# Optimization experiments

Hardware: AMD Instinct MI355X
Metric: run time of the kernel (lower is better)

## Reference

```python
import jax, jax.numpy as jnp
import numpy as np

T, IN, H, OUT = 4096, 2048, 2048, 1


def setup_inputs() -> dict:
    key = jax.random.key(0)
    ks = jax.random.split(key, 7)
    s = 0.02  # small init scale to keep gates in a sane range
    return {
        "x": jax.random.normal(ks[0], (T, 1, IN), dtype=jnp.float32),
        "W_ih": s * jax.random.normal(ks[1], (4 * H, IN), dtype=jnp.float32),
        "W_hh": s * jax.random.normal(ks[2], (4 * H, H), dtype=jnp.float32),
        "b_ih": s * jax.random.normal(ks[3], (4 * H,), dtype=jnp.float32),
        "b_hh": s * jax.random.normal(ks[4], (4 * H,), dtype=jnp.float32),
        "W_out": s * jax.random.normal(ks[5], (OUT, H), dtype=jnp.float32),
        "b_out": s * jax.random.normal(ks[6], (OUT,), dtype=jnp.float32),
    }


def reference(x, W_ih, W_hh, b_ih, b_hh, W_out, b_out):
    # Faithful LSTMCell loop (PyTorch gate order i, f, g, o) + per-step Linear.
    hidden = W_hh.shape[1]

    def step(carry, x_t):  # x_t: [1, IN]
        h, c = carry
        gates = x_t @ W_ih.T + b_ih + h @ W_hh.T + b_hh  # [1, 4H]
        i, f, g, o = jnp.split(gates, 4, axis=-1)
        i = jax.nn.sigmoid(i)
        f = jax.nn.sigmoid(f)
        g = jnp.tanh(g)
        o = jax.nn.sigmoid(o)
        c = f * c + i * g
        h = o * jnp.tanh(c)
        y = (h @ W_out.T + b_out)[0, 0]  # scalar, output_size == 1
        return (h, c), y

    h0 = jnp.zeros((1, hidden), dtype=x.dtype)
    c0 = jnp.zeros((1, hidden), dtype=x.dtype)
    _, res = jax.lax.scan(step, (h0, c0), x)
    return res  # [T]
```

## Files before the change

kernel.cpp:

```cpp
#include <hip/hip_runtime.h>

#define T_STEPS 4096
#define HD 2048
#define G4 8192
#define NWG 256
#define NTH 1024
#define SENT 0x7FC0DEADu

typedef __attribute__((ext_vector_type(8))) short bf16x8;
typedef __attribute__((ext_vector_type(4))) float f32x4;
typedef __attribute__((ext_vector_type(2))) float f32x2;
typedef __attribute__((ext_vector_type(8))) unsigned short u16x8;

static __device__ __forceinline__ unsigned short f2bf(float f){
  union { float f; unsigned int u; } v; v.f = f;
  unsigned int r = (v.u + 0x7fffu + ((v.u >> 16) & 1u)) >> 16;
  return (unsigned short)r;
}
static __device__ __forceinline__ float bf2f(unsigned short s){
  union { unsigned int u; float f; } v; v.u = ((unsigned int)s) << 16;
  return v.f;
}

static __device__ __forceinline__ f32x2 ld2_uc(const float* p){
  f32x2 r;
  asm volatile("global_load_dwordx2 %0, %1, off sc0 sc1\n\ts_waitcnt vmcnt(0)"
               : "=v"(r) : "v"(p) : "memory");
  return r;
}
static __device__ __forceinline__ void st_uc(float* p, float v){
  asm volatile("global_store_dword %0, %1, off sc0 sc1" :: "v"(p), "v"(v) : "memory");
}

__global__ void init_kernel(const float* __restrict__ b_ih, const float* __restrict__ b_hh,
                            float* __restrict__ bias, float* __restrict__ Hbuf){
  int i = blockIdx.x*blockDim.x + threadIdx.x;
  int stride = gridDim.x*blockDim.x;
  const int NTOT = G4 + (T_STEPS+1)*HD;
  union { unsigned int u; float f; } sent; sent.u = SENT;
  for (int idx = i; idx < NTOT; idx += stride){
    if (idx < G4) bias[idx] = b_ih[idx] + b_hh[idx];
    else {
      int j = idx - G4;
      Hbuf[j] = (j < HD) ? 0.f : sent.f;
    }
  }
}

__global__ __launch_bounds__(256) void gemm_xp(const float* __restrict__ X,
                                               const float* __restrict__ W,
                                               const float* __restrict__ bias,
                                               unsigned short* __restrict__ XP){
  __shared__ __align__(16) unsigned short As[128][40];
  __shared__ __align__(16) unsigned short Bs[128][40];
  const int tid = threadIdx.x;
  const int bx = blockIdx.x & 63;
  const int by = blockIdx.x >> 6;
  const int row0 = by*128, col0 = bx*128;
  const int l = tid & 63, w = tid >> 6;
  const int wrow = (w>>1)*64, wcol = (w&1)*64;
  const int lr = l & 15, lk = l >> 4;

  f32x4 acc[4][4];
  #pragma unroll
  for (int mi=0; mi<4; mi++)
    #pragma unroll
    for (int ni=0; ni<4; ni++)
      acc[mi][ni] = (f32x4){0.f,0.f,0.f,0.f};

  const int sr = tid >> 1;
  const int sh = (tid & 1) * 16;
  const float* xb = X + (size_t)(row0+sr)*2048 + sh;
  const float* wb = W + (size_t)(col0+sr)*2048 + sh;

  for (int k0 = 0; k0 < 2048; k0 += 32){
    __syncthreads();
    u16x8 va[2], vb[2];
    #pragma unroll
    for (int q=0; q<2; q++){
      float4 u = *(const float4*)(xb + k0 + q*8);
      float4 v = *(const float4*)(xb + k0 + q*8 + 4);
      u16x8 t;
      t[0]=f2bf(u.x); t[1]=f2bf(u.y); t[2]=f2bf(u.z); t[3]=f2bf(u.w);
      t[4]=f2bf(v.x); t[5]=f2bf(v.y); t[6]=f2bf(v.z); t[7]=f2bf(v.w);
      va[q]=t;
      float4 p = *(const float4*)(wb + k0 + q*8);
      float4 r = *(const float4*)(wb + k0 + q*8 + 4);
      u16x8 s;
      s[0]=f2bf(p.x); s[1]=f2bf(p.y); s[2]=f2bf(p.z); s[3]=f2bf(p.w);
      s[4]=f2bf(r.x); s[5]=f2bf(r.y); s[6]=f2bf(r.z); s[7]=f2bf(r.w);
      vb[q]=s;
    }
    *(u16x8*)&As[sr][sh]   = va[0];
    *(u16x8*)&As[sr][sh+8] = va[1];
    *(u16x8*)&Bs[sr][sh]   = vb[0];
    *(u16x8*)&Bs[sr][sh+8] = vb[1];
    __syncthreads();

    bf16x8 af[4], bfr[4];
    #pragma unroll
    for (int mi=0; mi<4; mi++) af[mi]  = *(const bf16x8*)&As[wrow+mi*16+lr][lk*8];
    #pragma unroll
    for (int ni=0; ni<4; ni++) bfr[ni] = *(const bf16x8*)&Bs[wcol+ni*16+lr][lk*8];
    #pragma unroll
    for (int mi=0; mi<4; mi++)
      #pragma unroll
      for (int ni=0; ni<4; ni++)
        acc[mi][ni] = __builtin_amdgcn_mfma_f32_16x16x32_bf16(af[mi], bfr[ni], acc[mi][ni], 0,0,0);
  }

  #pragma unroll
  for (int ni=0; ni<4; ni++){
    const int jc = col0 + wcol + ni*16 + lr;
    const float bv = bias[jc];
    #pragma unroll
    for (int mi=0; mi<4; mi++){
      const int tr0 = row0 + wrow + mi*16 + lk*4;
      #pragma unroll
      for (int r=0; r<4; r++)
        XP[(size_t)(tr0+r)*G4 + jc] = f2bf(acc[mi][ni][r] + bv);
    }
  }
}

__global__ __launch_bounds__(NTH, 4) void recur(const unsigned short* __restrict__ XP,
                                                const float* __restrict__ Whh,
                                                float* __restrict__ Hbuf){
  __shared__ float h_lds[HD];
  __shared__ float gsum[32];
  __shared__ float xp_s[32];
  const int g = blockIdx.x;
  const int tid = threadIdx.x;
  const int l = tid & 63, w = tid >> 6;

  float wv[2][8][4];
  #pragma unroll
  for (int ri=0; ri<2; ri++){
    const int rr = 2*w + ri;
    const size_t jrow = (size_t)(rr>>3)*HD + g*8 + (rr&7);
    const float* wp = Whh + jrow*HD + l*4;
    #pragma unroll
    for (int c=0; c<8; c++){
      float4 t4 = *(const float4*)(wp + c*256);
      wv[ri][c][0]=t4.x; wv[ri][c][1]=t4.y; wv[ri][c][2]=t4.z; wv[ri][c][3]=t4.w;
      asm volatile("" : "+v"(wv[ri][c][0]), "+v"(wv[ri][c][1]),
                        "+v"(wv[ri][c][2]), "+v"(wv[ri][c][3]));
    }
  }

  float c_reg = 0.f;

  for (int t=0; t<T_STEPS; ++t){
    if (tid < 32)
      xp_s[tid] = bf2f(XP[(size_t)t*G4 + (size_t)(tid>>3)*HD + g*8 + (tid&7)]);

    const float* hp = Hbuf + (size_t)t*HD + tid*2;
    f32x2 hv;
    do {
      hv = ld2_uc(hp);
    } while (__float_as_uint(hv[0]) == SENT || __float_as_uint(hv[1]) == SENT);
    *(f32x2*)&h_lds[tid*2] = hv;
    __syncthreads();

    float a0 = 0.f, a1 = 0.f;
    #pragma unroll
    for (int c=0; c<8; c++){
      float4 h4 = *(const float4*)&h_lds[c*256 + l*4];
      a0 += wv[0][c][0]*h4.x + wv[0][c][1]*h4.y + wv[0][c][2]*h4.z + wv[0][c][3]*h4.w;
      a1 += wv[1][c][0]*h4.x + wv[1][c][1]*h4.y + wv[1][c][2]*h4.z + wv[1][c][3]*h4.w;
    }
    #pragma unroll
    for (int off=32; off; off>>=1){
      a0 += __shfl_xor(a0, off, 64);
      a1 += __shfl_xor(a1, off, 64);
    }
    if (l == 0){ gsum[2*w] = a0; gsum[2*w+1] = a1; }
    __syncthreads();

    if (tid < 8){
      float ipre = gsum[tid]    + xp_s[tid];
      float fpre = gsum[8+tid]  + xp_s[8+tid];
      float gpre = gsum[16+tid] + xp_s[16+tid];
      float opre = gsum[24+tid] + xp_s[24+tid];
      float iv = 1.f/(1.f + __expf(-ipre));
      float fv = 1.f/(1.f + __expf(-fpre));
      float e2 = __expf(-2.f*gpre);
      float gv = (1.f - e2)/(1.f + e2);
      float ov = 1.f/(1.f + __expf(-opre));
      c_reg = fv*c_reg + iv*gv;
      float e2c = __expf(-2.f*c_reg);
      float th = (1.f - e2c)/(1.f + e2c);
      st_uc(Hbuf + (size_t)(t+1)*HD + g*8 + tid, ov*th);
    }
  }
}

__global__ __launch_bounds__(256) void out_gemv(const float* __restrict__ Hbuf,
                                                const float* __restrict__ Wout,
                                                const float* __restrict__ bout,
                                                float* __restrict__ y){
  const int t = blockIdx.x;
  const int tid = threadIdx.x;
  const float* h = Hbuf + (size_t)(t+1)*HD;
  float4 a0 = *(const float4*)(h + tid*8);
  float4 a1 = *(const float4*)(h + tid*8 + 4);
  float4 w0 = *(const float4*)(Wout + tid*8);
  float4 w1 = *(const float4*)(Wout + tid*8 + 4);
  float s = a0.x*w0.x + a0.y*w0.y + a0.z*w0.z + a0.w*w0.w
          + a1.x*w1.x + a1.y*w1.y + a1.z*w1.z + a1.w*w1.w;
  #pragma unroll
  for (int off=32; off; off>>=1) s += __shfl_xor(s, off, 64);
  __shared__ float ps[4];
  if ((tid & 63) == 0) ps[tid>>6] = s;
  __syncthreads();
  if (tid == 0) y[t] = ps[0]+ps[1]+ps[2]+ps[3] + bout[0];
}

extern "C" void kernel_launch(void* const* d_in, const int* in_sizes, int n_in,
                              void* d_out, int out_size, void* d_ws, size_t ws_size,
                              hipStream_t stream) {
  const float* x    = (const float*)d_in[0];
  const float* Wih  = (const float*)d_in[1];
  const float* Whh  = (const float*)d_in[2];
  const float* b_ih = (const float*)d_in[3];
  const float* b_hh = (const float*)d_in[4];
  const float* Wout = (const float*)d_in[5];
  const float* bout = (const float*)d_in[6];
  float* y = (float*)d_out;

  char* ws = (char*)d_ws;
  unsigned short* XP = (unsigned short*)(ws);
  float* Hbuf        = (float*)(ws + 67108864);
  float* bias        = (float*)(ws + 100671488);

  init_kernel<<<2048, 256, 0, stream>>>(b_ih, b_hh, bias, Hbuf);
  gemm_xp<<<2048, 256, 0, stream>>>(x, Wih, bias, XP);

  void* args[] = {(void*)&XP, (void*)&Whh, (void*)&Hbuf};
  hipLaunchCooperativeKernel((void*)recur, dim3(NWG), dim3(NTH), args, 0, stream);

  out_gemv<<<T_STEPS, 256, 0, stream>>>(Hbuf, Wout, bout, y);
}
```

Before: 10.53 ms.

## Store recurrent weights as bf16 in LDS instead of fp32 registers

```diff
diff --git a/kernel.cpp b/kernel.cpp
--- a/kernel.cpp
+++ b/kernel.cpp
@@ -6,6 +6,7 @@
 #define NWG 256
 #define NTH 1024
 #define SENT 0x7FC0DEADu
+#define SMEM_BYTES (131072 + 8192 + 128)
 
 typedef __attribute__((ext_vector_type(8))) short bf16x8;
 typedef __attribute__((ext_vector_type(4))) float f32x4;
@@ -20,6 +21,12 @@
 static __device__ __forceinline__ float bf2f(unsigned short s){
   union { unsigned int u; float f; } v; v.u = ((unsigned int)s) << 16;
   return v.f;
+}
+static __device__ __forceinline__ float blo(unsigned int u){
+  return __uint_as_float(u << 16);
+}
+static __device__ __forceinline__ float bhi(unsigned int u){
+  return __uint_as_float(u & 0xffff0000u);
 }
 
 static __device__ __forceinline__ f32x2 ld2_uc(const float* p){
@@ -126,34 +133,40 @@
 __global__ __launch_bounds__(NTH, 4) void recur(const unsigned short* __restrict__ XP,
                                                 const float* __restrict__ Whh,
                                                 float* __restrict__ Hbuf){
-  __shared__ float h_lds[HD];
-  __shared__ float gsum[32];
-  __shared__ float xp_s[32];
+  extern __shared__ char smem[];
+  float* h_lds = (float*)(smem + 131072);
+  float* gsum  = (float*)(smem + 131072 + 8192);
   const int g = blockIdx.x;
   const int tid = threadIdx.x;
   const int l = tid & 63, w = tid >> 6;
 
-  float wv[2][8][4];
   #pragma unroll
   for (int ri=0; ri<2; ri++){
     const int rr = 2*w + ri;
-    const size_t jrow = (size_t)(rr>>3)*HD + g*8 + (rr&7);
+    const size_t jrow = (size_t)(rr>>3)*HD + (size_t)g*8 + (rr&7);
     const float* wp = Whh + jrow*HD + l*4;
     #pragma unroll
-    for (int c=0; c<8; c++){
-      float4 t4 = *(const float4*)(wp + c*256);
-      wv[ri][c][0]=t4.x; wv[ri][c][1]=t4.y; wv[ri][c][2]=t4.z; wv[ri][c][3]=t4.w;
-      asm volatile("" : "+v"(wv[ri][c][0]), "+v"(wv[ri][c][1]),
-                        "+v"(wv[ri][c][2]), "+v"(wv[ri][c][3]));
+    for (int cp=0; cp<4; cp++){
+      float4 fa = *(const float4*)(wp + (2*cp)*256);
+      float4 fb = *(const float4*)(wp + (2*cp+1)*256);
+      uint4 pk;
+      pk.x = ((unsigned)f2bf(fa.y)<<16) | f2bf(fa.x);
+      pk.y = ((unsigned)f2bf(fa.w)<<16) | f2bf(fa.z);
+      pk.z = ((unsigned)f2bf(fb.y)<<16) | f2bf(fb.x);
+      pk.w = ((unsigned)f2bf(fb.w)<<16) | f2bf(fb.z);
+      *(uint4*)(smem + (size_t)((ri*4+cp)*1024 + tid)*16) = pk;
     }
   }
 
   float c_reg = 0.f;
+  float xpv[4] = {0,0,0,0};
 
   for (int t=0; t<T_STEPS; ++t){
-    if (tid < 32)
-      xp_s[tid] = bf2f(XP[(size_t)t*G4 + (size_t)(tid>>3)*HD + g*8 + (tid&7)]);
-
+    if (tid < 8){
+      #pragma unroll
+      for (int q=0; q<4; q++)
+        xpv[q] = bf2f(XP[(size_t)t*G4 + (size_t)q*HD + g*8 + tid]);
+    }
     const float* hp = Hbuf + (size_t)t*HD + tid*2;
     f32x2 hv;
     do {
@@ -164,10 +177,15 @@
 
     float a0 = 0.f, a1 = 0.f;
     #pragma unroll
-    for (int c=0; c<8; c++){
-      float4 h4 = *(const float4*)&h_lds[c*256 + l*4];
-      a0 += wv[0][c][0]*h4.x + wv[0][c][1]*h4.y + wv[0][c][2]*h4.z + wv[0][c][3]*h4.w;
-      a1 += wv[1][c][0]*h4.x + wv[1][c][1]*h4.y + wv[1][c][2]*h4.z + wv[1][c][3]*h4.w;
+    for (int cp=0; cp<4; cp++){
+      float4 ha = *(const float4*)&h_lds[(2*cp)*256 + l*4];
+      float4 hb = *(const float4*)&h_lds[(2*cp+1)*256 + l*4];
+      uint4 w0 = *(const uint4*)(smem + (size_t)((cp  )*1024 + tid)*16);
+      uint4 w1 = *(const uint4*)(smem + (size_t)((4+cp)*1024 + tid)*16);
+      a0 += blo(w0.x)*ha.x + bhi(w0.x)*ha.y + blo(w0.y)*ha.z + bhi(w0.y)*ha.w
+          + blo(w0.z)*hb.x + bhi(w0.z)*hb.y + blo(w0.w)*hb.z + bhi(w0.w)*hb.w;
+      a1 += blo(w1.x)*ha.x + bhi(w1.x)*ha.y + blo(w1.y)*ha.z + bhi(w1.y)*ha.w
+          + blo(w1.z)*hb.x + bhi(w1.z)*hb.y + blo(w1.w)*hb.z + bhi(w1.w)*hb.w;
     }
     #pragma unroll
     for (int off=32; off; off>>=1){
@@ -178,10 +196,10 @@
     __syncthreads();
 
     if (tid < 8){
-      float ipre = gsum[tid]    + xp_s[tid];
-      float fpre = gsum[8+tid]  + xp_s[8+tid];
-      float gpre = gsum[16+tid] + xp_s[16+tid];
-      float opre = gsum[24+tid] + xp_s[24+tid];
+      float ipre = gsum[tid]    + xpv[0];
+      float fpre = gsum[8+tid]  + xpv[1];
+      float gpre = gsum[16+tid] + xpv[2];
+      float opre = gsum[24+tid] + xpv[3];
       float iv = 1.f/(1.f + __expf(-ipre));
       float fv = 1.f/(1.f + __expf(-fpre));
       float e2 = __expf(-2.f*gpre);
@@ -236,8 +254,11 @@
   init_kernel<<<2048, 256, 0, stream>>>(b_ih, b_hh, bias, Hbuf);
   gemm_xp<<<2048, 256, 0, stream>>>(x, Wih, bias, XP);
 
+  hipFuncSetAttribute((const void*)recur,
+                      hipFuncAttributeMaxDynamicSharedMemorySize, SMEM_BYTES);
   void* args[] = {(void*)&XP, (void*)&Whh, (void*)&Hbuf};
-  hipLaunchCooperativeKernel((void*)recur, dim3(NWG), dim3(NTH), args, 0, stream);
+  hipLaunchCooperativeKernel((void*)recur, dim3(NWG), dim3(NTH), args,
+                             SMEM_BYTES, stream);
 
   out_gemv<<<T_STEPS, 256, 0, stream>>>(Hbuf, Wout, bout, y);
 }
```

After: 11.90 ms. +12.9%, slower.
